# Kernel tuning notes

Measured on AMD Instinct MI355X. Metric: run time of the kernel, lower is better.

Reference implementation:

```python
import jax, jax.numpy as jnp
import numpy as np
import math

B, T, N, D = 8, 12, 500, 512  # batch, time(heads), nodes, K*d
FACTOR = 5
SAMPLE_K = min(FACTOR * math.ceil(math.log(N)), N)  # = 35, also n_top (N_Q == N_K)
W_SCALE = 0.02


def setup_inputs() -> dict:
    key = jax.random.key(0)
    ks = jax.random.split(key, 9)
    f32 = jnp.float32
    return {
        "X":   jax.random.normal(ks[0], (B, T, N, D), f32),
        "STE": jax.random.normal(ks[1], (B, T, N, D), f32),
        "Wq":  jax.random.normal(ks[2], (2 * D, D), f32) * W_SCALE,
        "bq":  jnp.zeros((D,), f32),
        "Wk":  jax.random.normal(ks[3], (2 * D, D), f32) * W_SCALE,
        "bk":  jnp.zeros((D,), f32),
        "Wv":  jax.random.normal(ks[4], (2 * D, D), f32) * W_SCALE,
        "bv":  jnp.zeros((D,), f32),
        "sample_idx": jax.random.randint(ks[5], (N, SAMPLE_K), 0, N, jnp.int32),
    }


def reference(X, STE, Wq, bq, Wk, bk, Wv, bv, sample_idx):
    # concat spatial features with spatio-temporal embedding -> projections
    Xc = jnp.concatenate([X, STE], axis=-1)                  # [B,T,N,2D]
    q = jax.nn.relu(Xc @ Wq + bq)                            # [B,T,N,D]
    k = jax.nn.relu(Xc @ Wk + bk)
    v = jax.nn.relu(Xc @ Wv + bv)

    n_top = SAMPLE_K
    # _prob_QK: sampled Q-K scores. Since SAMPLE_K*D >> N, computing the full
    # [B,T,N,N] score matrix and gathering the sampled columns is strictly
    # cheaper in memory than materializing K_sample [B,T,N,S,D] as torch does;
    # the math (Q_K_sample values) is identical.
    scores_full = jnp.einsum('bhld,bhmd->bhlm', q, k)        # [B,T,N,N]
    QK_sample = jnp.take_along_axis(
        scores_full, sample_idx[None, None, :, :], axis=3)   # [B,T,N,S]
    # sparsity measure M = max - mean (mean over L_K = N)
    M = QK_sample.max(axis=-1) - QK_sample.sum(axis=-1) / N  # [B,T,N]
    _, idx = jax.lax.top_k(M, n_top)                         # [B,T,n_top]

    # reduced-query full attention scores (gather rows of full scores == Q_reduce @ K^T)
    scores = jnp.take_along_axis(scores_full, idx[..., None], axis=2)  # [B,T,u,N]
    scores = scores * (1.0 / math.sqrt(D))

    # ProbMask (mask_flag=True): causal mask per selected query position
    j = jnp.arange(N)
    mask = j[None, None, None, :] > idx[..., None]           # [B,T,u,N]
    scores = jnp.where(mask, -jnp.inf, scores)
    attn = jax.nn.softmax(scores, axis=-1)                   # [B,T,u,N]
    ctx_new = jnp.einsum('bhun,bhnd->bhud', attn, v)         # [B,T,u,D]

    # initial context = causal cumsum of V, then scatter-update selected queries
    context = jnp.cumsum(v, axis=2)                          # [B,T,N,D]
    bi = jnp.arange(B)[:, None, None]
    hi = jnp.arange(T)[None, :, None]
    context = context.at[bi, hi, idx].set(ctx_new)
    # .transpose(2,1) in torch -> swap axes 1 and 2
    return context.transpose(0, 2, 1, 3)                     # [B,N,T,D]
```

## Files before the change

kernel.cpp:

```cpp
#include <hip/hip_runtime.h>
#include <math.h>

#define B_    8
#define T_    12
#define BT    96
#define NN    500
#define DD    512
#define KK    1024
#define SK    35
#define MROWS 48000

typedef __bf16 bf16x8 __attribute__((ext_vector_type(8)));
typedef float f32x4 __attribute__((ext_vector_type(4)));
typedef unsigned short u16;
typedef u16 ushort8_t __attribute__((ext_vector_type(8)));
typedef u16 ushort4_t __attribute__((ext_vector_type(4)));

__device__ __forceinline__ u16 bf_hi(float x) {
  __bf16 h = (__bf16)x;
  return __builtin_bit_cast(u16, h);
}
__device__ __forceinline__ float bf_tof(u16 b) {
  unsigned int u = ((unsigned int)b) << 16;
  return __builtin_bit_cast(float, u);
}

__global__ __launch_bounds__(256) void convW_kernel(
    const float* __restrict__ W, u16* __restrict__ Bth, u16* __restrict__ Btl)
{
  const int n = blockIdx.x;
  const int k0 = threadIdx.x * 4;
  float xs[4];
#pragma unroll
  for (int j = 0; j < 4; ++j) xs[j] = W[(size_t)(k0 + j) * 512 + n];
  ushort4_t hi, lo;
#pragma unroll
  for (int j = 0; j < 4; ++j) {
    u16 h = bf_hi(xs[j]);
    hi[j] = h;
    lo[j] = bf_hi(xs[j] - bf_tof(h));
  }
  *(ushort4_t*)(Bth + (size_t)n * 1024 + k0) = hi;
  *(ushort4_t*)(Btl + (size_t)n * 1024 + k0) = lo;
}

template<int PASSES>
__global__ __launch_bounds__(256) void mfma_proj(
    const float* __restrict__ X, const float* __restrict__ STE,
    const u16* __restrict__ Bth, const u16* __restrict__ Btl,
    const float* __restrict__ bias, float* __restrict__ out)
{
  constexpr int NT = (PASSES == 3) ? 2 : 1;
  __shared__ u16 ldsbuf[NT * 4096];
  u16* lAh = ldsbuf;
  u16* lAl = ldsbuf + ((NT == 2) ? 4096 : 0);
  const int tid = threadIdx.x;
  const int lane = tid & 63;
  const int wid = tid >> 6;
  const int wm = wid >> 1, wn = wid & 1;
  const int orig = blockIdx.x;
  const int xcd = orig & 7, pos = orig >> 3;
  const int wg = (xcd < 4 ? xcd * 188 : 752 + (xcd - 4) * 187) + pos;
  const int r0 = (wg >> 2) * 128;
  const int c0 = (wg & 3) * 128;
  const int fr = lane & 15, fk = lane >> 4;

  f32x4 acc[4][4];
#pragma unroll
  for (int m = 0; m < 4; ++m)
#pragma unroll
    for (int n = 0; n < 4; ++n) acc[m][n] = f32x4{0.f, 0.f, 0.f, 0.f};

  const size_t bfo = (size_t)(c0 + wn * 64 + fr) * 1024 + fk * 8;

  for (int kt = 0; kt < 32; ++kt) {
    const int kk0 = kt * 32;
    bf16x8 bh[4], bl[4];
#pragma unroll
    for (int n = 0; n < 4; ++n) {
      const size_t go = bfo + (size_t)n * 16 * 1024 + kk0;
      bh[n] = *(const bf16x8*)(Bth + go);
      if (PASSES == 3) bl[n] = *(const bf16x8*)(Btl + go);
    }
#pragma unroll
    for (int p = 0; p < 2; ++p) {
      const int c = tid + p * 256;
      const int row = c >> 2, kc = c & 3;
      const int dst = row * 32 + ((kc ^ ((row >> 1) & 3)) * 8);
      const int col = kk0 + kc * 8;
      const float* src = (col < 512)
          ? (X + (size_t)(r0 + row) * 512 + col)
          : (STE + (size_t)(r0 + row) * 512 + (col - 512));
      float4 x0 = *(const float4*)src;
      float4 x1 = *(const float4*)(src + 4);
      float xs[8] = {x0.x, x0.y, x0.z, x0.w, x1.x, x1.y, x1.z, x1.w};
      ushort8_t hi, lo;
#pragma unroll
      for (int j = 0; j < 8; ++j) {
        u16 h = bf_hi(xs[j]);
        hi[j] = h;
        if (PASSES == 3) lo[j] = bf_hi(xs[j] - bf_tof(h));
      }
      *(ushort8_t*)&lAh[dst] = hi;
      if (PASSES == 3) *(ushort8_t*)&lAl[dst] = lo;
    }
    __syncthreads();
    bf16x8 ah[4], al[4];
#pragma unroll
    for (int m = 0; m < 4; ++m) {
      const int row = wm * 64 + m * 16 + fr;
      const int off = row * 32 + ((fk ^ ((row >> 1) & 3)) * 8);
      ah[m] = *(const bf16x8*)&lAh[off];
      if (PASSES == 3) al[m] = *(const bf16x8*)&lAl[off];
    }
#pragma unroll
    for (int m = 0; m < 4; ++m)
#pragma unroll
      for (int n = 0; n < 4; ++n) {
        acc[m][n] = __builtin_amdgcn_mfma_f32_16x16x32_bf16(
            ah[m], bh[n], acc[m][n], 0, 0, 0);
        if (PASSES == 3) {
          acc[m][n] = __builtin_amdgcn_mfma_f32_16x16x32_bf16(
              ah[m], bl[n], acc[m][n], 0, 0, 0);
          acc[m][n] = __builtin_amdgcn_mfma_f32_16x16x32_bf16(
              al[m], bh[n], acc[m][n], 0, 0, 0);
        }
      }
    __syncthreads();
  }
#pragma unroll
  for (int n = 0; n < 4; ++n) {
    const int col = c0 + wn * 64 + n * 16 + fr;
    const float bb = bias[col];
#pragma unroll
    for (int m = 0; m < 4; ++m) {
      const int rowb = r0 + wm * 64 + m * 16 + fk * 4;
#pragma unroll
      for (int r = 0; r < 4; ++r)
        out[(size_t)(rowb + r) * 512 + col] = fmaxf(acc[m][n][r] + bb, 0.f);
    }
  }
}

__global__ __launch_bounds__(256) void sampled_M_kernel(
    const float* __restrict__ q, const float* __restrict__ k,
    const int* __restrict__ sidx, float* __restrict__ Mout)
{
  const int tid = threadIdx.x;
  const int lane = tid & 63, wid = tid >> 6;
  const int bid = blockIdx.x;
  const int xcd = bid & 7, j = bid >> 3;
  const int btg = j / 125, ub = j - btg * 125;
  const int bt = btg * 8 + xcd;
  const int nn = ub * 4 + wid;
  const int n = bt * NN + nn;
  const float* qrow = q + (size_t)n * DD + lane * 8;
  float4 q0 = *(const float4*)qrow;
  float4 q1 = *(const float4*)(qrow + 4);
  const float* kbase = k + (size_t)bt * NN * DD;
  float mx = -INFINITY, sm = 0.f;
  for (int s = 0; s < SK; ++s) {
    int m = sidx[nn * SK + s];
    const float* krow = kbase + (size_t)m * DD + lane * 8;
    float4 k0 = *(const float4*)krow;
    float4 k1 = *(const float4*)(krow + 4);
    float ss = q0.x*k0.x + q0.y*k0.y + q0.z*k0.z + q0.w*k0.w
             + q1.x*k1.x + q1.y*k1.y + q1.z*k1.z + q1.w*k1.w;
#pragma unroll
    for (int off = 32; off > 0; off >>= 1) ss += __shfl_xor(ss, off);
    mx = fmaxf(mx, ss);
    sm += ss;
  }
  if (lane == 0) Mout[n] = mx - sm * (1.0f / (float)NN);
}

__global__ __launch_bounds__(256) void topk_kernel(
    const float* __restrict__ Mb, int* __restrict__ idxb,
    int* __restrict__ sqi, int* __restrict__ su)
{
  const int bt = blockIdx.x;
  const int tid = threadIdx.x;
  __shared__ float mv[NN];
  __shared__ float rv[256];
  __shared__ int ri[256];
  __shared__ int qsel[SK];
  for (int n = tid; n < NN; n += 256) mv[n] = Mb[(size_t)bt * NN + n];
  __syncthreads();
  for (int it = 0; it < SK; ++it) {
    float bv = -INFINITY; int bi = NN;
    for (int n = tid; n < NN; n += 256) {
      float x = mv[n];
      if (x > bv) { bv = x; bi = n; }
    }
    rv[tid] = bv; ri[tid] = bi;
    __syncthreads();
    for (int sft = 128; sft > 0; sft >>= 1) {
      if (tid < sft) {
        float xv = rv[tid + sft]; int xi = ri[tid + sft];
        if (xv > rv[tid] || (xv == rv[tid] && xi < ri[tid])) {
          rv[tid] = xv; ri[tid] = xi;
        }
      }
      __syncthreads();
    }
    if (tid == 0) {
      idxb[bt * SK + it] = ri[0];
      qsel[it] = ri[0];
      mv[ri[0]] = -INFINITY;
    }
    __syncthreads();
  }
  if (tid < SK) {
    int myqi = qsel[tid];
    int rank = 0;
    for (int j = 0; j < SK; ++j) rank += (qsel[j] < myqi);
    sqi[bt * SK + rank] = myqi;
    su[bt * SK + rank] = tid;
  }
}

__global__ __launch_bounds__(256) void attn_part_kernel(
    const float* __restrict__ q, const float* __restrict__ k,
    const float* __restrict__ v, const int* __restrict__ sqi,
    float* __restrict__ pO, float* __restrict__ pm, float* __restrict__ pl)
{
  const int bid = blockIdx.x;
  const int xcd = bid & 7, j = bid >> 3;
  const int btg = j / 35, rem = j - btg * 35;
  const int g = rem / 5, c = rem % 5;
  const int bt = btg * 8 + xcd;
  const int base = bt * SK + g * 5;
  const int c0 = c * 100;
  const int tid = threadIdx.x;
  const int lane = tid & 63, wid = tid >> 6;

  __shared__ float sc[5][100];
  __shared__ int qg[5];
  __shared__ float pmx[5], psm[5];
  if (tid < 5) qg[tid] = sqi[base + tid];
  __syncthreads();
  const int gq = qg[4];
  const int mend = (gq < c0 + 99) ? gq : (c0 + 99);

  float4 qr[5][2];
#pragma unroll
  for (int jj = 0; jj < 5; ++jj) {
    const float* qp = q + ((size_t)bt * NN + qg[jj]) * DD + lane * 8;
    qr[jj][0] = *(const float4*)qp;
    qr[jj][1] = *(const float4*)(qp + 4);
  }
  const float scale = 0.044194173824159216f;

  for (int m = c0 + wid; m <= mend; m += 4) {
    const float* krow = k + ((size_t)bt * NN + m) * DD + lane * 8;
    float4 k0 = *(const float4*)krow;
    float4 k1 = *(const float4*)(krow + 4);
    float p[5];
#pragma unroll
    for (int jj = 0; jj < 5; ++jj) {
      p[jj] = qr[jj][0].x*k0.x + qr[jj][0].y*k0.y
            + qr[jj][0].z*k0.z + qr[jj][0].w*k0.w
            + qr[jj][1].x*k1.x + qr[jj][1].y*k1.y
            + qr[jj][1].z*k1.z + qr[jj][1].w*k1.w;
    }
#pragma unroll
    for (int off = 32; off > 0; off >>= 1)
#pragma unroll
      for (int jj = 0; jj < 5; ++jj) p[jj] += __shfl_xor(p[jj], off);
    if (lane == 0) {
#pragma unroll
      for (int jj = 0; jj < 5; ++jj) sc[jj][m - c0] = p[jj] * scale;
    }
  }
  __syncthreads();

  for (int jj = wid; jj < 5; jj += 4) {
    const int qe = (qg[jj] < c0 + 99) ? qg[jj] : (c0 + 99);
    const int len = qe - c0 + 1;
    float mx = -3e38f;
    for (int i = lane; i < len; i += 64) mx = fmaxf(mx, sc[jj][i]);
#pragma unroll
    for (int off = 32; off > 0; off >>= 1) mx = fmaxf(mx, __shfl_xor(mx, off));
    float sm = 0.f;
    for (int i = lane; i < len; i += 64) {
      float e = __expf(sc[jj][i] - mx);
      sc[jj][i] = e;
      sm += e;
    }
#pragma unroll
    for (int off = 32; off > 0; off >>= 1) sm += __shfl_xor(sm, off);
    if (lane == 0) { pmx[jj] = mx; psm[jj] = sm; }
  }
  __syncthreads();

  float a0[5] = {0.f,0.f,0.f,0.f,0.f}, a1[5] = {0.f,0.f,0.f,0.f,0.f};
  const float* vb = v + (size_t)bt * NN * DD;
  for (int m = c0; m <= mend; ++m) {
    float v0 = vb[(size_t)m * DD + tid];
    float v1 = vb[(size_t)m * DD + tid + 256];
#pragma unroll
    for (int jj = 0; jj < 5; ++jj) {
      if (m <= qg[jj]) {
        float w = sc[jj][m - c0];
        a0[jj] = fmaf(w, v0, a0[jj]);
        a1[jj] = fmaf(w, v1, a1[jj]);
      }
    }
  }

  const int pidx = (bt * 7 + g) * 5 + c;
  if (tid < 5) {
    pm[pidx * 5 + tid] = pmx[tid];
    pl[pidx * 5 + tid] = psm[tid];
  }
#pragma unroll
  for (int jj = 0; jj < 5; ++jj) {
    float* po = pO + ((size_t)(pidx * 5 + jj)) * DD;
    po[tid] = a0[jj];
    po[tid + 256] = a1[jj];
  }
}

__global__ __launch_bounds__(512) void attn_combine_kernel(
    const float* __restrict__ pO, const float* __restrict__ pm,
    const float* __restrict__ pl, const int* __restrict__ su,
    float* __restrict__ ctxn)
{
  const int bid = blockIdx.x;
  const int bt = bid / SK, s = bid % SK;
  const int g = s / 5, jj = s % 5;
  const int d = threadIdx.x;
  __shared__ float w[5];
  __shared__ float linv;
  if (d == 0) {
    float m_[5], l_[5], mx = -3e38f;
#pragma unroll
    for (int c = 0; c < 5; ++c) {
      const int pidx = (bt * 7 + g) * 5 + c;
      m_[c] = pm[pidx * 5 + jj];
      l_[c] = pl[pidx * 5 + jj];
      mx = fmaxf(mx, m_[c]);
    }
    float lt = 0.f;
#pragma unroll
    for (int c = 0; c < 5; ++c) {
      float wc = __expf(m_[c] - mx);
      w[c] = wc;
      lt += wc * l_[c];
    }
    linv = 1.f / lt;
  }
  __syncthreads();
  float o = 0.f;
#pragma unroll
  for (int c = 0; c < 5; ++c) {
    const int pidx = (bt * 7 + g) * 5 + c;
    o = fmaf(w[c], pO[((size_t)(pidx * 5 + jj)) * DD + d], o);
  }
  const int u = su[bt * SK + s];
  ctxn[((size_t)bt * SK + u) * DD + d] = o * linv;
}

__global__ __launch_bounds__(512) void vchunk_sum_kernel(
    const float* __restrict__ v, float* __restrict__ csum)
{
  const int ch = blockIdx.x, bt = blockIdx.y;
  const int d = threadIdx.x;
  const float* vb = v + ((size_t)bt * NN + ch * 50) * DD + d;
  float s = 0.f;
  for (int n = 0; n < 50; ++n) s += vb[(size_t)n * DD];
  csum[((size_t)bt * 10 + ch) * DD + d] = s;
}

__global__ __launch_bounds__(512) void cumsum_scatter2_kernel(
    const float* __restrict__ v, const int* __restrict__ idxb,
    const float* __restrict__ ctxn, const float* __restrict__ csum,
    float* __restrict__ out)
{
  const int ch = blockIdx.x, bt = blockIdx.y;
  const int b = bt / T_, t = bt % T_;
  const int d = threadIdx.x;
  const int n0 = ch * 50;
  __shared__ int sel[50];
  if (threadIdx.x < 50) sel[threadIdx.x] = -1;
  __syncthreads();
  if (threadIdx.x < SK) {
    int qi = idxb[bt * SK + threadIdx.x];
    if (qi >= n0 && qi < n0 + 50) sel[qi - n0] = threadIdx.x;
  }
  __syncthreads();
  float s = 0.f;
  for (int c = 0; c < ch; ++c) s += csum[((size_t)bt * 10 + c) * DD + d];
  for (int i = 0; i < 50; ++i) {
    s += v[((size_t)bt * NN + n0 + i) * DD + d];
    float o = s;
    int u = sel[i];
    if (u >= 0) o = ctxn[((size_t)bt * SK + u) * DD + d];
    out[(((size_t)b * NN + (n0 + i)) * T_ + t) * DD + d] = o;
  }
}

extern "C" void kernel_launch(void* const* d_in, const int* in_sizes, int n_in,
                              void* d_out, int out_size, void* d_ws, size_t ws_size,
                              hipStream_t stream) {
  const float* X   = (const float*)d_in[0];
  const float* STE = (const float*)d_in[1];
  const float* Wq  = (const float*)d_in[2];
  const float* bq  = (const float*)d_in[3];
  const float* Wk  = (const float*)d_in[4];
  const float* bk  = (const float*)d_in[5];
  const float* Wv  = (const float*)d_in[6];
  const float* bv  = (const float*)d_in[7];
  const int* sidx  = (const int*)d_in[8];
  float* out = (float*)d_out;

  float* q    = (float*)d_ws;
  float* k    = q + (size_t)MROWS * DD;
  float* v    = k + (size_t)MROWS * DD;
  float* Mb   = v + (size_t)MROWS * DD;
  int*   idxb = (int*)(Mb + MROWS);
  float* ctxn = (float*)(idxb + BT * SK);
  u16* Bqh = (u16*)(ctxn + (size_t)BT * SK * DD);
  u16* Bql = Bqh + (size_t)512 * 1024;
  u16* Bkh = Bql + (size_t)512 * 1024;
  u16* Bkl = Bkh + (size_t)512 * 1024;
  u16* Bvh = Bkl + (size_t)512 * 1024;
  u16* Bvl = Bvh + (size_t)512 * 1024;
  float* csum = (float*)Bqh;
  int*   sqi  = (int*)Bkh;
  int*   su   = sqi + BT * SK;
  float* pm   = (float*)(su + BT * SK);
  float* pl   = pm + 3360 * 5;
  float* pO   = (float*)d_out;
  (void)ws_size; (void)in_sizes; (void)n_in; (void)out_size;

  convW_kernel<<<512, 256, 0, stream>>>(Wq, Bqh, Bql);
  convW_kernel<<<512, 256, 0, stream>>>(Wk, Bkh, Bkl);
  convW_kernel<<<512, 256, 0, stream>>>(Wv, Bvh, Bvl);

  mfma_proj<3><<<1500, 256, 0, stream>>>(X, STE, Bqh, Bql, bq, q);
  mfma_proj<3><<<1500, 256, 0, stream>>>(X, STE, Bkh, Bkl, bk, k);
  mfma_proj<1><<<1500, 256, 0, stream>>>(X, STE, Bvh, Bvl, bv, v);

  sampled_M_kernel<<<12000, 256, 0, stream>>>(q, k, sidx, Mb);
  topk_kernel<<<BT, 256, 0, stream>>>(Mb, idxb, sqi, su);
  attn_part_kernel<<<3360, 256, 0, stream>>>(q, k, v, sqi, pO, pm, pl);
  attn_combine_kernel<<<3360, 512, 0, stream>>>(pO, pm, pl, su, ctxn);
  dim3 g5(10, BT);
  vchunk_sum_kernel<<<g5, 512, 0, stream>>>(v, csum);
  cumsum_scatter2_kernel<<<g5, 512, 0, stream>>>(v, idxb, ctxn, csum, out);
}
```

Before: 1.048 ms.

## Fuse Q and K projections into one kernel and stage weights through LDS

The Q and K projection GEMMs are merged into one kernel. It reads and splits each X/STE tile into hi/lo bf16 once and accumulates both outputs, which halves the activation traffic and conversion work for those two projections. Weight tiles for all projections are now staged cooperatively into swizzled LDS instead of each wave loading them directly from global memory. The cost is double the accumulator registers (32 f32x4 per thread), about 48KB of LDS per block, and possibly lower occupancy or register spills.

```diff
diff --git a/kernel.cpp b/kernel.cpp
--- a/kernel.cpp
+++ b/kernel.cpp
@@ -25,6 +25,10 @@
   return __builtin_bit_cast(float, u);
 }
 
+__device__ __forceinline__ int lds_off(int row, int kq) {
+  return row * 32 + ((kq ^ ((row >> 1) & 3)) * 8);
+}
+
 __global__ __launch_bounds__(256) void convW_kernel(
     const float* __restrict__ W, u16* __restrict__ Bth, u16* __restrict__ Btl)
 {
@@ -44,16 +48,19 @@
   *(ushort4_t*)(Btl + (size_t)n * 1024 + k0) = lo;
 }
 
-template<int PASSES>
-__global__ __launch_bounds__(256) void mfma_proj(
+__global__ __launch_bounds__(256) void mfma_proj_qk(
     const float* __restrict__ X, const float* __restrict__ STE,
-    const u16* __restrict__ Bth, const u16* __restrict__ Btl,
-    const float* __restrict__ bias, float* __restrict__ out)
-{
-  constexpr int NT = (PASSES == 3) ? 2 : 1;
-  __shared__ u16 ldsbuf[NT * 4096];
-  u16* lAh = ldsbuf;
-  u16* lAl = ldsbuf + ((NT == 2) ? 4096 : 0);
+    const u16* __restrict__ Bqh_, const u16* __restrict__ Bql_,
+    const u16* __restrict__ Bkh_, const u16* __restrict__ Bkl_,
+    const float* __restrict__ bq, const float* __restrict__ bk,
+    float* __restrict__ qout, float* __restrict__ kout)
+{
+  __shared__ u16 lAh[4096];
+  __shared__ u16 lAl[4096];
+  __shared__ u16 lBqh[4096];
+  __shared__ u16 lBql[4096];
+  __shared__ u16 lBkh[4096];
+  __shared__ u16 lBkl[4096];
   const int tid = threadIdx.x;
   const int lane = tid & 63;
   const int wid = tid >> 6;
@@ -65,28 +72,22 @@
   const int c0 = (wg & 3) * 128;
   const int fr = lane & 15, fk = lane >> 4;
 
-  f32x4 acc[4][4];
+  f32x4 accq[4][4], acck[4][4];
 #pragma unroll
   for (int m = 0; m < 4; ++m)
 #pragma unroll
-    for (int n = 0; n < 4; ++n) acc[m][n] = f32x4{0.f, 0.f, 0.f, 0.f};
-
-  const size_t bfo = (size_t)(c0 + wn * 64 + fr) * 1024 + fk * 8;
+    for (int n = 0; n < 4; ++n) {
+      accq[m][n] = f32x4{0.f, 0.f, 0.f, 0.f};
+      acck[m][n] = f32x4{0.f, 0.f, 0.f, 0.f};
+    }
 
   for (int kt = 0; kt < 32; ++kt) {
     const int kk0 = kt * 32;
-    bf16x8 bh[4], bl[4];
-#pragma unroll
-    for (int n = 0; n < 4; ++n) {
-      const size_t go = bfo + (size_t)n * 16 * 1024 + kk0;
-      bh[n] = *(const bf16x8*)(Bth + go);
-      if (PASSES == 3) bl[n] = *(const bf16x8*)(Btl + go);
-    }
 #pragma unroll
     for (int p = 0; p < 2; ++p) {
       const int c = tid + p * 256;
       const int row = c >> 2, kc = c & 3;
-      const int dst = row * 32 + ((kc ^ ((row >> 1) & 3)) * 8);
+      const int dst = lds_off(row, kc);
       const int col = kk0 + kc * 8;
       const float* src = (col < 512)
           ? (X + (size_t)(r0 + row) * 512 + col)
@@ -99,45 +100,136 @@
       for (int j = 0; j < 8; ++j) {
         u16 h = bf_hi(xs[j]);
         hi[j] = h;
-        if (PASSES == 3) lo[j] = bf_hi(xs[j] - bf_tof(h));
+        lo[j] = bf_hi(xs[j] - bf_tof(h));
       }
       *(ushort8_t*)&lAh[dst] = hi;
-      if (PASSES == 3) *(ushort8_t*)&lAl[dst] = lo;
+      *(ushort8_t*)&lAl[dst] = lo;
+      const size_t gb = (size_t)(c0 + row) * 1024 + kk0 + kc * 8;
+      *(ushort8_t*)&lBqh[dst] = *(const ushort8_t*)(Bqh_ + gb);
+      *(ushort8_t*)&lBql[dst] = *(const ushort8_t*)(Bql_ + gb);
+      *(ushort8_t*)&lBkh[dst] = *(const ushort8_t*)(Bkh_ + gb);
+      *(ushort8_t*)&lBkl[dst] = *(const ushort8_t*)(Bkl_ + gb);
     }
     __syncthreads();
     bf16x8 ah[4], al[4];
 #pragma unroll
     for (int m = 0; m < 4; ++m) {
-      const int row = wm * 64 + m * 16 + fr;
-      const int off = row * 32 + ((fk ^ ((row >> 1) & 3)) * 8);
+      const int off = lds_off(wm * 64 + m * 16 + fr, fk);
       ah[m] = *(const bf16x8*)&lAh[off];
-      if (PASSES == 3) al[m] = *(const bf16x8*)&lAl[off];
-    }
-#pragma unroll
-    for (int m = 0; m < 4; ++m)
-#pragma unroll
-      for (int n = 0; n < 4; ++n) {
-        acc[m][n] = __builtin_amdgcn_mfma_f32_16x16x32_bf16(
-            ah[m], bh[n], acc[m][n], 0, 0, 0);
-        if (PASSES == 3) {
-          acc[m][n] = __builtin_amdgcn_mfma_f32_16x16x32_bf16(
-              ah[m], bl[n], acc[m][n], 0, 0, 0);
-          acc[m][n] = __builtin_amdgcn_mfma_f32_16x16x32_bf16(
-              al[m], bh[n], acc[m][n], 0, 0, 0);
-        }
+      al[m] = *(const bf16x8*)&lAl[off];
+    }
+#pragma unroll
+    for (int n = 0; n < 4; ++n) {
+      const int off = lds_off(wn * 64 + n * 16 + fr, fk);
+      bf16x8 bqh = *(const bf16x8*)&lBqh[off];
+      bf16x8 bql = *(const bf16x8*)&lBql[off];
+      bf16x8 bkh = *(const bf16x8*)&lBkh[off];
+      bf16x8 bkl = *(const bf16x8*)&lBkl[off];
+#pragma unroll
+      for (int m = 0; m < 4; ++m) {
+        accq[m][n] = __builtin_amdgcn_mfma_f32_16x16x32_bf16(
+            ah[m], bqh, accq[m][n], 0, 0, 0);
+        acck[m][n] = __builtin_amdgcn_mfma_f32_16x16x32_bf16(
+            ah[m], bkh, acck[m][n], 0, 0, 0);
+        accq[m][n] = __builtin_amdgcn_mfma_f32_16x16x32_bf16(
+            ah[m], bql, accq[m][n], 0, 0, 0);
+        acck[m][n] = __builtin_amdgcn_mfma_f32_16x16x32_bf16(
+            ah[m], bkl, acck[m][n], 0, 0, 0);
+        accq[m][n] = __builtin_amdgcn_mfma_f32_16x16x32_bf16(
+            al[m], bqh, accq[m][n], 0, 0, 0);
+        acck[m][n] = __builtin_amdgcn_mfma_f32_16x16x32_bf16(
+            al[m], bkh, acck[m][n], 0, 0, 0);
       }
+    }
     __syncthreads();
   }
 #pragma unroll
   for (int n = 0; n < 4; ++n) {
     const int col = c0 + wn * 64 + n * 16 + fr;
-    const float bb = bias[col];
+    const float bbq = bq[col];
+    const float bbk = bk[col];
 #pragma unroll
     for (int m = 0; m < 4; ++m) {
       const int rowb = r0 + wm * 64 + m * 16 + fk * 4;
 #pragma unroll
+      for (int r = 0; r < 4; ++r) {
+        qout[(size_t)(rowb + r) * 512 + col] = fmaxf(accq[m][n][r] + bbq, 0.f);
+        kout[(size_t)(rowb + r) * 512 + col] = fmaxf(acck[m][n][r] + bbk, 0.f);
+      }
+    }
+  }
+}
+
+__global__ __launch_bounds__(256) void mfma_proj_v(
+    const float* __restrict__ X, const float* __restrict__ STE,
+    const u16* __restrict__ Bvh_, const float* __restrict__ bv,
+    float* __restrict__ vout)
+{
+  __shared__ u16 lAh[4096];
+  __shared__ u16 lBh[4096];
+  const int tid = threadIdx.x;
+  const int lane = tid & 63;
+  const int wid = tid >> 6;
+  const int wm = wid >> 1, wn = wid & 1;
+  const int orig = blockIdx.x;
+  const int xcd = orig & 7, pos = orig >> 3;
+  const int wg = (xcd < 4 ? xcd * 188 : 752 + (xcd - 4) * 187) + pos;
+  const int r0 = (wg >> 2) * 128;
+  const int c0 = (wg & 3) * 128;
+  const int fr = lane & 15, fk = lane >> 4;
+
+  f32x4 acc[4][4];
+#pragma unroll
+  for (int m = 0; m < 4; ++m)
+#pragma unroll
+    for (int n = 0; n < 4; ++n) acc[m][n] = f32x4{0.f, 0.f, 0.f, 0.f};
+
+  for (int kt = 0; kt < 32; ++kt) {
+    const int kk0 = kt * 32;
+#pragma unroll
+    for (int p = 0; p < 2; ++p) {
+      const int c = tid + p * 256;
+      const int row = c >> 2, kc = c & 3;
+      const int dst = lds_off(row, kc);
+      const int col = kk0 + kc * 8;
+      const float* src = (col < 512)
+          ? (X + (size_t)(r0 + row) * 512 + col)
+          : (STE + (size_t)(r0 + row) * 512 + (col - 512));
+      float4 x0 = *(const float4*)src;
+      float4 x1 = *(const float4*)(src + 4);
+      float xs[8] = {x0.x, x0.y, x0.z, x0.w, x1.x, x1.y, x1.z, x1.w};
+      ushort8_t hi;
+#pragma unroll
+      for (int j = 0; j < 8; ++j) hi[j] = bf_hi(xs[j]);
+      *(ushort8_t*)&lAh[dst] = hi;
+      const size_t gb = (size_t)(c0 + row) * 1024 + kk0 + kc * 8;
+      *(ushort8_t*)&lBh[dst] = *(const ushort8_t*)(Bvh_ + gb);
+    }
+    __syncthreads();
+    bf16x8 ah[4];
+#pragma unroll
+    for (int m = 0; m < 4; ++m)
+      ah[m] = *(const bf16x8*)&lAh[lds_off(wm * 64 + m * 16 + fr, fk)];
+#pragma unroll
+    for (int n = 0; n < 4; ++n) {
+      bf16x8 bh = *(const bf16x8*)&lBh[lds_off(wn * 64 + n * 16 + fr, fk)];
+#pragma unroll
+      for (int m = 0; m < 4; ++m)
+        acc[m][n] = __builtin_amdgcn_mfma_f32_16x16x32_bf16(
+            ah[m], bh, acc[m][n], 0, 0, 0);
+    }
+    __syncthreads();
+  }
+#pragma unroll
+  for (int n = 0; n < 4; ++n) {
+    const int col = c0 + wn * 64 + n * 16 + fr;
+    const float bb = bv[col];
+#pragma unroll
+    for (int m = 0; m < 4; ++m) {
+      const int rowb = r0 + wm * 64 + m * 16 + fk * 4;
+#pragma unroll
       for (int r = 0; r < 4; ++r)
-        out[(size_t)(rowb + r) * 512 + col] = fmaxf(acc[m][n][r] + bb, 0.f);
+        vout[(size_t)(rowb + r) * 512 + col] = fmaxf(acc[m][n][r] + bb, 0.f);
     }
   }
 }
@@ -438,9 +530,9 @@
   convW_kernel<<<512, 256, 0, stream>>>(Wk, Bkh, Bkl);
   convW_kernel<<<512, 256, 0, stream>>>(Wv, Bvh, Bvl);
 
-  mfma_proj<3><<<1500, 256, 0, stream>>>(X, STE, Bqh, Bql, bq, q);
-  mfma_proj<3><<<1500, 256, 0, stream>>>(X, STE, Bkh, Bkl, bk, k);
-  mfma_proj<1><<<1500, 256, 0, stream>>>(X, STE, Bvh, Bvl, bv, v);
+  mfma_proj_qk<<<1500, 256, 0, stream>>>(X, STE, Bqh, Bql, Bkh, Bkl,
+                                         bq, bk, q, k);
+  mfma_proj_v<<<1500, 256, 0, stream>>>(X, STE, Bvh, bv, v);
 
   sampled_M_kernel<<<12000, 256, 0, stream>>>(q, k, sidx, Mb);
   topk_kernel<<<BT, 256, 0, stream>>>(Mb, idxb, sqi, su);
```

Result: faster. 1.019 ms (-2.8%).
